# Kernel tuning notes

Hardware: AMD Instinct MI355X
Metric: run time of the kernel (lower is better)

## Reference

```python
import jax, jax.numpy as jnp
import numpy as np

N = 10000      # nodes
E = 640000     # edges (avg degree 64)
D = 128        # embedding_size
L = 3          # num_layers=4 -> 1 + (4-2) = 3 conv layers


def setup_inputs() -> dict:
    key = jax.random.key(0)
    ks = jax.random.split(key, 4)
    z = jax.random.normal(ks[0], (N, D), dtype=jnp.float32)
    edge_index = jax.random.randint(ks[1], (2, E), 0, N, dtype=jnp.int32)
    # per-layer GCN weights/bias and LayerNorm affine params, stacked over layers
    Ws = jax.random.normal(ks[2], (L, D, D), dtype=jnp.float32) / np.sqrt(D).astype(np.float32)
    bs = jnp.zeros((L, D), dtype=jnp.float32)
    gammas = jnp.ones((L, D), dtype=jnp.float32)
    betas = jnp.zeros((L, D), dtype=jnp.float32)
    return {"z": z, "edge_index": edge_index, "Ws": Ws, "bs": bs,
            "gammas": gammas, "betas": betas}


def _layernorm(x, g, b, eps=1e-5):
    mu = jnp.mean(x, axis=-1, keepdims=True)
    var = jnp.var(x, axis=-1, keepdims=True)
    return (x - mu) * jax.lax.rsqrt(var + eps) * g + b


def reference(z, edge_index, Ws, bs, gammas, betas):
    # GCNConv (PyG default): add self-loops, symmetric normalization
    loops = jnp.arange(N, dtype=edge_index.dtype)
    src = jnp.concatenate([edge_index[0], loops])   # [E+N]
    dst = jnp.concatenate([edge_index[1], loops])   # [E+N]
    deg = jax.ops.segment_sum(jnp.ones(src.shape[0], z.dtype), dst, num_segments=N)
    dinv = jax.lax.rsqrt(jnp.maximum(deg, 1.0))
    norm = dinv[src] * dinv[dst]                    # [E+N]

    x = z
    for i in range(L):
        xw = x @ Ws[i]                              # [N, D] dense transform
        msg = xw[src] * norm[:, None]               # gather + scale  [E+N, D]
        x = jax.ops.segment_sum(msg, dst, num_segments=N) + bs[i]  # scatter-add
        x = _layernorm(x, gammas[i], betas[i])
        x = jax.nn.gelu(x)
        # F.dropout(p=0.1) omitted: deterministic eval-mode reference
    return x
```

## Files before the change

### kernel.cpp

```cpp
#include <hip/hip_runtime.h>

#define DD 128
#define D2 64
#define BW_DST 32
#define BW_SHIFT 5
#define BATCH 4096
#define NBPAD 320
#define P2CAP 6144

struct alignas(8) Rec { unsigned int meta; float w; };

__device__ __forceinline__ unsigned int bf16rne(float f) {
    unsigned int u = __float_as_uint(f);
    unsigned int r = ((u >> 16) & 1u) + 0x7fffu;
    return (u + r) >> 16;
}
__device__ __forceinline__ float bflo(unsigned int v) { return __uint_as_float(v << 16); }
__device__ __forceinline__ float bfhi(unsigned int v) { return __uint_as_float(v & 0xFFFF0000u); }


__global__ __launch_bounds__(256) void bucket_count(
    const int* __restrict__ dst, int E, int* __restrict__ bsum, int NB)
{
    __shared__ int cnt[NBPAD];
    int t = threadIdx.x;
    for (int b = t; b < NB; b += 256) cnt[b] = 0;
    __syncthreads();
    int gtid = blockIdx.x * 256 + t, gsz = gridDim.x * 256;
    for (int e = gtid; e < E; e += gsz) atomicAdd(&cnt[dst[e] >> BW_SHIFT], 1);
    __syncthreads();
    for (int b = t; b < NB; b += 256) if (cnt[b]) atomicAdd(&bsum[b], cnt[b]);
}

__global__ void scan_bsum(const int* __restrict__ bsum, int* __restrict__ bbase,
                          int* __restrict__ bcur, int* __restrict__ row_ptr,
                          int NB, int N, int E)
{
    __shared__ int part[256];
    int t = threadIdx.x;
    int chunk = (NB + 255) / 256;
    int lo = t * chunk, hi = min(lo + chunk, NB);
    int s = 0;
    for (int b = lo; b < hi; ++b) s += bsum[b];
    part[t] = s;
    __syncthreads();
    for (int o = 1; o < 256; o <<= 1) {
        int v = (t >= o) ? part[t - o] : 0;
        __syncthreads();
        part[t] += v;
        __syncthreads();
    }
    int run = (t == 0) ? 0 : part[t - 1];
    for (int b = lo; b < hi; ++b) {
        bbase[b] = run;
        bcur[b] = run;
        run += bsum[b];
    }
    if (t == 0) row_ptr[N] = E;
}

__global__ __launch_bounds__(256) void bucket_fill(
    const int* __restrict__ src, const int* __restrict__ dst, int E,
    int* __restrict__ bcur, unsigned int* __restrict__ bcsr, int NB)
{
    __shared__ unsigned short sbkt[BATCH];
    __shared__ int cnt[NBPAD];
    __shared__ int boff[NBPAD + 1];
    __shared__ int gbase[NBPAD];
    __shared__ int lcur[NBPAD];
    __shared__ unsigned int staged[BATCH];
    __shared__ int wpart[256];
    int t = threadIdx.x;

    for (int base = blockIdx.x * BATCH; base < E; base += gridDim.x * BATCH) {
        int n = min(E - base, BATCH);
        for (int b = t; b < NB; b += 256) cnt[b] = 0;
        __syncthreads();
        for (int i = t; i < n; i += 256) {
            int d = dst[base + i];
            int bk = d >> BW_SHIFT;
            sbkt[i] = (unsigned short)bk;
            atomicAdd(&cnt[bk], 1);
        }
        __syncthreads();
        int chunk = (NB + 255) / 256;
        int lo = t * chunk, hi = min(lo + chunk, NB);
        int s = 0;
        for (int b = lo; b < hi; ++b) s += cnt[b];
        wpart[t] = s;
        __syncthreads();
        for (int o = 1; o < 256; o <<= 1) {
            int v = (t >= o) ? wpart[t - o] : 0;
            __syncthreads();
            wpart[t] += v;
            __syncthreads();
        }
        int run = (t == 0) ? 0 : wpart[t - 1];
        for (int b = lo; b < hi; ++b) {
            boff[b] = run;
            lcur[b] = run;
            if (cnt[b] > 0) gbase[b] = atomicAdd(&bcur[b], cnt[b]);
            run += cnt[b];
        }
        if (t == 0) boff[NB] = n;
        __syncthreads();
        for (int i = t; i < n; i += 256) {
            int e = base + i;
            int ss = src[e], dd = dst[e];
            int bk = sbkt[i];
            int p = atomicAdd(&lcur[bk], 1);
            staged[p] = (unsigned int)ss | ((unsigned int)(dd & (BW_DST - 1)) << 27);
        }
        __syncthreads();
        int wid = t >> 6, lane = t & 63;
        for (int b = wid; b < NB; b += 4) {
            int s0 = boff[b];
            int c = boff[b + 1] - s0;
            if (c == 0) continue;
            int g = gbase[b];
            for (int j = lane; j < c; j += 64) bcsr[g + j] = staged[s0 + j];
        }
        __syncthreads();
    }
}

__global__ __launch_bounds__(256) void fine_sort(
    const int* __restrict__ bbase, const unsigned int* __restrict__ bcsr,
    unsigned int* __restrict__ csr4, int* __restrict__ row_ptr,
    float* __restrict__ dinv, int N, int NB, int E)
{
    __shared__ unsigned int staged[P2CAP];
    __shared__ int dcnt[BW_DST];
    __shared__ int dcur[BW_DST];
    int b = blockIdx.x;
    int d0 = b << BW_SHIFT;
    int nd = min(BW_DST, N - d0);
    int base = bbase[b];
    int end  = (b + 1 < NB) ? bbase[b + 1] : E;
    int cnt  = end - base;
    int t = threadIdx.x;
    if (t < BW_DST) dcnt[t] = 0;
    __syncthreads();
    for (int i = t; i < cnt; i += 256) atomicAdd(&dcnt[bcsr[base + i] >> 27], 1);
    __syncthreads();
    if (t < BW_DST) {
        int c = dcnt[t];
        int v = c;
        #pragma unroll
        for (int o = 1; o < BW_DST; o <<= 1) { int u = __shfl_up(v, o, BW_DST); if (t >= o) v += u; }
        int loff = v - c;
        if (t < nd) {
            int node = d0 + t;
            row_ptr[node] = base + loff;
            dinv[node] = rsqrtf((float)(c + 1));
        }
        dcur[t] = loff;
    }
    __syncthreads();
    if (cnt <= P2CAP) {
        for (int i = t; i < cnt; i += 256) {
            unsigned int r = bcsr[base + i];
            int p = atomicAdd(&dcur[r >> 27], 1);
            staged[p] = r;
        }
        __syncthreads();
        for (int i = t; i < cnt; i += 256) csr4[base + i] = staged[i];
    } else {
        for (int i = t; i < cnt; i += 256) {
            unsigned int r = bcsr[base + i];
            int p = atomicAdd(&dcur[r >> 27], 1);
            csr4[base + p] = r;
        }
    }
}

__global__ __launch_bounds__(256) void weight_fill(
    const int* __restrict__ bbase, const unsigned int* __restrict__ csr4,
    const float* __restrict__ dinv, Rec* __restrict__ csr, int NB, int N, int E)
{
    int b = blockIdx.x;
    int base = bbase[b];
    int end  = (b + 1 < NB) ? bbase[b + 1] : E;
    int d0 = b << BW_SHIFT;
    for (int i = base + threadIdx.x; i < end; i += 256) {
        unsigned int r = csr4[i];
        int s = r & 0x07FFFFFFu;
        int d = d0 + (int)(r >> 27);
        Rec rec;
        rec.meta = r;
        rec.w = dinv[s] * dinv[d];
        csr[i] = rec;
    }
}


#define GR 16
__global__ void gemm_xw(const float* __restrict__ x, const float* __restrict__ W,
                        unsigned int* __restrict__ xwb, int N) {
    __shared__ float xs[GR][DD];
    int t = threadIdx.x;
    int r0 = blockIdx.x * GR;
    #pragma unroll
    for (int r = 0; r < GR; ++r) {
        int row = r0 + r;
        xs[r][t] = (row < N) ? x[row * DD + t] : 0.f;
    }
    __syncthreads();
    float acc[GR];
    #pragma unroll
    for (int r = 0; r < GR; ++r) acc[r] = 0.f;
    for (int k = 0; k < DD; k += 4) {
        float w0 = W[(k + 0) * DD + t];
        float w1 = W[(k + 1) * DD + t];
        float w2 = W[(k + 2) * DD + t];
        float w3 = W[(k + 3) * DD + t];
        #pragma unroll
        for (int r = 0; r < GR; ++r) {
            float4 xv = *(const float4*)&xs[r][k];
            acc[r] = fmaf(xv.x, w0, acc[r]);
            acc[r] = fmaf(xv.y, w1, acc[r]);
            acc[r] = fmaf(xv.z, w2, acc[r]);
            acc[r] = fmaf(xv.w, w3, acc[r]);
        }
    }
    #pragma unroll
    for (int r = 0; r < GR; ++r) {
        int row = r0 + r;
        float other = __shfl_xor(acc[r], 1);
        if (row < N && !(t & 1)) {
            unsigned int p = bf16rne(acc[r]) | (bf16rne(other) << 16);
            xwb[row * D2 + (t >> 1)] = p;
        }
    }
}

__global__ __launch_bounds__(512) void agg_gemm(
    const unsigned int* __restrict__ xwb_in, const Rec* __restrict__ csr,
    const int* __restrict__ row_ptr, const float* __restrict__ dinv,
    const float* __restrict__ bias, const float* __restrict__ gamma,
    const float* __restrict__ beta, const float* __restrict__ W,
    unsigned int* __restrict__ xwb_out, int N)
{
    __shared__ float xs[8][DD];
    int t = threadIdx.x;
    int wid = t >> 6, l = t & 63;
    int i = blockIdx.x * 8 + wid;
    if (i < N) {
        int beg = row_ptr[i], end = row_ptr[i + 1];
        float ax = 0.f, ay = 0.f;
        #pragma unroll 4
        for (int j = beg; j < end; ++j) {
            Rec er = csr[j];
            unsigned int v = xwb_in[(er.meta & 0x07FFFFFFu) * D2 + l];
            ax = fmaf(bflo(v), er.w, ax);
            ay = fmaf(bfhi(v), er.w, ay);
        }
        float di = dinv[i], sn = di * di;
        unsigned int v = xwb_in[i * D2 + l];
        ax = fmaf(bflo(v), sn, ax);
        ay = fmaf(bfhi(v), sn, ay);
        float2 b2 = ((const float2*)bias)[l];
        ax += b2.x; ay += b2.y;
        float sum = ax + ay, sq = ax * ax + ay * ay;
        #pragma unroll
        for (int o = 32; o > 0; o >>= 1) { sum += __shfl_xor(sum, o); sq += __shfl_xor(sq, o); }
        float mu   = sum * (1.f / DD);
        float var  = sq * (1.f / DD) - mu * mu;
        float rstd = rsqrtf(var + 1e-5f);
        float2 g2  = ((const float2*)gamma)[l];
        float2 be2 = ((const float2*)beta)[l];
        float y0 = (ax - mu) * rstd * g2.x + be2.x;
        float y1 = (ay - mu) * rstd * g2.y + be2.y;
        y0 = 0.5f * y0 * (1.f + tanhf(0.7978845608f * (y0 + 0.044715f * y0 * y0 * y0)));
        y1 = 0.5f * y1 * (1.f + tanhf(0.7978845608f * (y1 + 0.044715f * y1 * y1 * y1)));
        xs[wid][2 * l]     = y0;
        xs[wid][2 * l + 1] = y1;
    } else {
        xs[wid][2 * l]     = 0.f;
        xs[wid][2 * l + 1] = 0.f;
    }
    __syncthreads();
    int col = t & 127, h = t >> 7;
    float a0 = 0.f, a1 = 0.f;
    for (int k = 0; k < DD; k += 4) {
        float w0 = W[(k + 0) * DD + col];
        float w1 = W[(k + 1) * DD + col];
        float w2 = W[(k + 2) * DD + col];
        float w3 = W[(k + 3) * DD + col];
        float4 x0 = *(const float4*)&xs[h * 2 + 0][k];
        float4 x1 = *(const float4*)&xs[h * 2 + 1][k];
        a0 = fmaf(x0.x, w0, a0); a0 = fmaf(x0.y, w1, a0);
        a0 = fmaf(x0.z, w2, a0); a0 = fmaf(x0.w, w3, a0);
        a1 = fmaf(x1.x, w0, a1); a1 = fmaf(x1.y, w1, a1);
        a1 = fmaf(x1.z, w2, a1); a1 = fmaf(x1.w, w3, a1);
    }
    int row0 = blockIdx.x * 8 + h * 2;
    float o0 = __shfl_xor(a0, 1);
    float o1 = __shfl_xor(a1, 1);
    if (!(t & 1)) {
        if (row0 < N)
            xwb_out[row0 * D2 + (col >> 1)] = bf16rne(a0) | (bf16rne(o0) << 16);
        if (row0 + 1 < N)
            xwb_out[(row0 + 1) * D2 + (col >> 1)] = bf16rne(a1) | (bf16rne(o1) << 16);
    }
}

__global__ void agg_ln_gelu(const unsigned int* __restrict__ xwb, const Rec* __restrict__ csr,
                            const int* __restrict__ row_ptr, const float* __restrict__ dinv,
                            const float* __restrict__ bias, const float* __restrict__ gamma,
                            const float* __restrict__ beta, float* __restrict__ out) {
    int i = blockIdx.x;
    int l = threadIdx.x;
    int beg = row_ptr[i], end = row_ptr[i + 1];
    float ax = 0.f, ay = 0.f;
    #pragma unroll 4
    for (int j = beg; j < end; ++j) {
        Rec er = csr[j];
        unsigned int v = xwb[(er.meta & 0x07FFFFFFu) * D2 + l];
        ax = fmaf(bflo(v), er.w, ax);
        ay = fmaf(bfhi(v), er.w, ay);
    }
    float di = dinv[i], sn = di * di;
    unsigned int v = xwb[i * D2 + l];
    ax = fmaf(bflo(v), sn, ax);
    ay = fmaf(bfhi(v), sn, ay);
    float2 b2 = ((const float2*)bias)[l];
    ax += b2.x; ay += b2.y;
    float sum = ax + ay, sq = ax * ax + ay * ay;
    #pragma unroll
    for (int o = 32; o > 0; o >>= 1) { sum += __shfl_xor(sum, o); sq += __shfl_xor(sq, o); }
    float mu   = sum * (1.f / DD);
    float var  = sq * (1.f / DD) - mu * mu;
    float rstd = rsqrtf(var + 1e-5f);
    float2 g2  = ((const float2*)gamma)[l];
    float2 be2 = ((const float2*)beta)[l];
    float y0 = (ax - mu) * rstd * g2.x + be2.x;
    float y1 = (ay - mu) * rstd * g2.y + be2.y;
    y0 = 0.5f * y0 * (1.f + tanhf(0.7978845608f * (y0 + 0.044715f * y0 * y0 * y0)));
    y1 = 0.5f * y1 * (1.f + tanhf(0.7978845608f * (y1 + 0.044715f * y1 * y1 * y1)));
    float2 o2; o2.x = y0; o2.y = y1;
    ((float2*)out)[i * D2 + l] = o2;
}

static inline size_t align_up(size_t x, size_t a) { return (x + a - 1) & ~(a - 1); }

extern "C" void kernel_launch(void* const* d_in, const int* in_sizes, int n_in,
                              void* d_out, int out_size, void* d_ws, size_t ws_size,
                              hipStream_t stream) {
    const float* z      = (const float*)d_in[0];
    const int*   ei     = (const int*)d_in[1];
    const float* Ws     = (const float*)d_in[2];
    const float* bs     = (const float*)d_in[3];
    const float* gammas = (const float*)d_in[4];
    const float* betas  = (const float*)d_in[5];

    int E  = in_sizes[1] / 2;
    int LD = in_sizes[3];
    int Dd = in_sizes[2] / LD;
    int L  = LD / Dd;
    int N  = in_sizes[0] / Dd;
    int NB = (N + BW_DST - 1) / BW_DST;

    const int* srcp = ei;
    const int* dstp = ei + E;

    char* ws = (char*)d_ws;
    size_t off = 0;
    int* bsum = (int*)(ws + off);        off = align_up(off + (size_t)NBPAD * 4, 256);
    int* bbase = (int*)(ws + off);       off = align_up(off + (size_t)NBPAD * 4, 256);
    int* bcur = (int*)(ws + off);        off = align_up(off + (size_t)NBPAD * 4, 256);
    float* dinv = (float*)(ws + off);    off = align_up(off + (size_t)N * 4, 256);
    int* row_ptr = (int*)(ws + off);     off = align_up(off + (size_t)(N + 1) * 4, 256);
    unsigned int* bcsr = (unsigned int*)(ws + off); off = align_up(off + (size_t)E * 4, 256);
    unsigned int* csr4 = (unsigned int*)(ws + off); off = align_up(off + (size_t)E * 4, 256);
    Rec* csr = (Rec*)(ws + off);         off = align_up(off + (size_t)E * 8, 256);
    unsigned int* xwb_a = (unsigned int*)(ws + off); off = align_up(off + (size_t)N * D2 * 4, 256);
    unsigned int* xwb_b = (unsigned int*)(ws + off); off = align_up(off + (size_t)N * D2 * 4, 256);
    float* dout = (float*)d_out;
    (void)ws_size; (void)n_in; (void)out_size;

    int nb_p1 = (E + BATCH - 1) / BATCH;

    hipMemsetAsync(bsum, 0, (size_t)NBPAD * 4, stream);
    bucket_count<<<160, 256, 0, stream>>>(dstp, E, bsum, NB);
    scan_bsum<<<1, 256, 0, stream>>>(bsum, bbase, bcur, row_ptr, NB, N, E);
    bucket_fill<<<nb_p1, 256, 0, stream>>>(srcp, dstp, E, bcur, bcsr, NB);
    fine_sort<<<NB, 256, 0, stream>>>(bbase, bcsr, csr4, row_ptr, dinv, N, NB, E);
    weight_fill<<<NB, 256, 0, stream>>>(bbase, csr4, dinv, csr, NB, N, E);

    gemm_xw<<<(N + GR - 1) / GR, DD, 0, stream>>>(z, Ws, xwb_a, N);

    unsigned int* tin = xwb_a;
    unsigned int* tout = xwb_b;
    for (int li = 0; li < L - 1; ++li) {
        agg_gemm<<<(N + 7) / 8, 512, 0, stream>>>(
            tin, csr, row_ptr, dinv,
            bs + (size_t)li * Dd, gammas + (size_t)li * Dd, betas + (size_t)li * Dd,
            Ws + (size_t)(li + 1) * Dd * Dd, tout, N);
        unsigned int* tmp = tin; tin = tout; tout = tmp;
    }

    agg_ln_gelu<<<N, 64, 0, stream>>>(tin, csr, row_ptr, dinv,
                                      bs + (size_t)(L - 1) * Dd,
                                      gammas + (size_t)(L - 1) * Dd,
                                      betas + (size_t)(L - 1) * Dd, dout);
}
```

Before: 174.9 us.

## Use wave-level scan in bucket_fill, halve batch, and pack final aggregation blocks

```diff
diff --git a/kernel.cpp b/kernel.cpp
--- a/kernel.cpp
+++ b/kernel.cpp
@@ -4,7 +4,7 @@
 #define D2 64
 #define BW_DST 32
 #define BW_SHIFT 5
-#define BATCH 4096
+#define BATCH 2048
 #define NBPAD 320
 #define P2CAP 6144
 
@@ -69,12 +69,11 @@
     __shared__ int gbase[NBPAD];
     __shared__ int lcur[NBPAD];
     __shared__ unsigned int staged[BATCH];
-    __shared__ int wpart[256];
     int t = threadIdx.x;
 
     for (int base = blockIdx.x * BATCH; base < E; base += gridDim.x * BATCH) {
         int n = min(E - base, BATCH);
-        for (int b = t; b < NB; b += 256) cnt[b] = 0;
+        for (int b = t; b < NBPAD; b += 256) cnt[b] = 0;
         __syncthreads();
         for (int i = t; i < n; i += 256) {
             int d = dst[base + i];
@@ -83,26 +82,27 @@
             atomicAdd(&cnt[bk], 1);
         }
         __syncthreads();
-        int chunk = (NB + 255) / 256;
-        int lo = t * chunk, hi = min(lo + chunk, NB);
-        int s = 0;
-        for (int b = lo; b < hi; ++b) s += cnt[b];
-        wpart[t] = s;
-        __syncthreads();
-        for (int o = 1; o < 256; o <<= 1) {
-            int v = (t >= o) ? wpart[t - o] : 0;
-            __syncthreads();
-            wpart[t] += v;
-            __syncthreads();
-        }
-        int run = (t == 0) ? 0 : wpart[t - 1];
-        for (int b = lo; b < hi; ++b) {
-            boff[b] = run;
-            lcur[b] = run;
-            if (cnt[b] > 0) gbase[b] = atomicAdd(&bcur[b], cnt[b]);
-            run += cnt[b];
-        }
-        if (t == 0) boff[NB] = n;
+        if (t < 64) {
+            int lo = t * 5;
+            int c0 = cnt[lo], c1 = cnt[lo + 1], c2 = cnt[lo + 2],
+                c3 = cnt[lo + 3], c4 = cnt[lo + 4];
+            int s = c0 + c1 + c2 + c3 + c4;
+            int v = s;
+            #pragma unroll
+            for (int o = 1; o < 64; o <<= 1) { int u = __shfl_up(v, o, 64); if (t >= o) v += u; }
+            int e0 = v - s;
+            int e1 = e0 + c0, e2 = e1 + c1, e3 = e2 + c2, e4 = e3 + c3;
+            boff[lo] = e0; boff[lo + 1] = e1; boff[lo + 2] = e2;
+            boff[lo + 3] = e3; boff[lo + 4] = e4;
+            lcur[lo] = e0; lcur[lo + 1] = e1; lcur[lo + 2] = e2;
+            lcur[lo + 3] = e3; lcur[lo + 4] = e4;
+            if (c0) gbase[lo]     = atomicAdd(&bcur[lo],     c0);
+            if (c1) gbase[lo + 1] = atomicAdd(&bcur[lo + 1], c1);
+            if (c2) gbase[lo + 2] = atomicAdd(&bcur[lo + 2], c2);
+            if (c3) gbase[lo + 3] = atomicAdd(&bcur[lo + 3], c3);
+            if (c4) gbase[lo + 4] = atomicAdd(&bcur[lo + 4], c4);
+            if (t == 63) boff[NBPAD] = n;
+        }
         __syncthreads();
         for (int i = t; i < n; i += 256) {
             int e = base + i;
@@ -248,7 +248,7 @@
     if (i < N) {
         int beg = row_ptr[i], end = row_ptr[i + 1];
         float ax = 0.f, ay = 0.f;
-        #pragma unroll 4
+        #pragma unroll 8
         for (int j = beg; j < end; ++j) {
             Rec er = csr[j];
             unsigned int v = xwb_in[(er.meta & 0x07FFFFFFu) * D2 + l];
@@ -305,15 +305,18 @@
     }
 }
 
-__global__ void agg_ln_gelu(const unsigned int* __restrict__ xwb, const Rec* __restrict__ csr,
-                            const int* __restrict__ row_ptr, const float* __restrict__ dinv,
-                            const float* __restrict__ bias, const float* __restrict__ gamma,
-                            const float* __restrict__ beta, float* __restrict__ out) {
-    int i = blockIdx.x;
-    int l = threadIdx.x;
+__global__ __launch_bounds__(256) void agg_ln_gelu(
+    const unsigned int* __restrict__ xwb, const Rec* __restrict__ csr,
+    const int* __restrict__ row_ptr, const float* __restrict__ dinv,
+    const float* __restrict__ bias, const float* __restrict__ gamma,
+    const float* __restrict__ beta, float* __restrict__ out, int N)
+{
+    int i = blockIdx.x * 4 + (threadIdx.x >> 6);
+    if (i >= N) return;
+    int l = threadIdx.x & 63;
     int beg = row_ptr[i], end = row_ptr[i + 1];
     float ax = 0.f, ay = 0.f;
-    #pragma unroll 4
+    #pragma unroll 8
     for (int j = beg; j < end; ++j) {
         Rec er = csr[j];
         unsigned int v = xwb[(er.meta & 0x07FFFFFFu) * D2 + l];
@@ -400,8 +403,8 @@
         unsigned int* tmp = tin; tin = tout; tout = tmp;
     }
 
-    agg_ln_gelu<<<N, 64, 0, stream>>>(tin, csr, row_ptr, dinv,
-                                      bs + (size_t)(L - 1) * Dd,
-                                      gammas + (size_t)(L - 1) * Dd,
-                                      betas + (size_t)(L - 1) * Dd, dout);
-}
+    agg_ln_gelu<<<(N + 3) / 4, 256, 0, stream>>>(tin, csr, row_ptr, dinv,
+                                                 bs + (size_t)(L - 1) * Dd,
+                                                 gammas + (size_t)(L - 1) * Dd,
+                                                 betas + (size_t)(L - 1) * Dd, dout, N);
+}
```

New measurement: 192.9 us. 1.1x slower.
